# Performance work log

Hardware: AMD Instinct MI355X
Metric: run time of the kernel (lower is better)

Reference implementation:

```python
import jax, jax.numpy as jnp
import numpy as np

STD = 0.01

def setup_inputs() -> dict:
    key = jax.random.key(0)
    k1, k2, k3 = jax.random.split(key, 3)
    B, T, D = 16, 4096, 512
    x = jax.random.normal(k1, (B, T, D), dtype=jnp.float32)
    att_W = jax.random.normal(k2, (D, D), dtype=jnp.float32) * STD
    att_v = jax.random.normal(k3, (D,), dtype=jnp.float32) * STD
    return {"x": x, "att_W": att_W, "att_v": att_v}

def reference(x, att_W, att_v):
    # additive attention scores: tanh(x @ W) @ v -> [B, T]
    y = jnp.tanh(jnp.einsum('btd,de->bte', x, att_W))
    scores = jnp.einsum('btd,d->bt', y, att_v)
    weights = jax.nn.softmax(scores, axis=-1)          # softmax over sequence
    out = jnp.einsum('bt,btd->bd', weights, x)         # weighted sum pooling
    return out.astype(jnp.float32)
```

## Files before the change

### kernel.cpp

```cpp
#include <hip/hip_runtime.h>
#include <hip/hip_bf16.h>
#include <math.h>

#define BB 16
#define TT 4096
#define DD 512
#define MM (BB*TT)

typedef __bf16 bf16x8 __attribute__((ext_vector_type(8)));
typedef float  f32x4  __attribute__((ext_vector_type(4)));

__device__ inline unsigned short f2bf(float f) {
    unsigned u = __builtin_bit_cast(unsigned, f) + 0x8000u;
    return (unsigned short)(u >> 16);
}

__device__ inline unsigned pack_bf16x2(float lo, float hi) {
    unsigned u0 = __builtin_bit_cast(unsigned, lo) + 0x8000u;
    unsigned u1 = __builtin_bit_cast(unsigned, hi) + 0x8000u;
    return __builtin_amdgcn_perm(u1, u0, 0x07060302);
}

__device__ inline float tanh_fast(float y) {
    float e = __expf(2.0f * y);
    return 1.0f - 2.0f * __builtin_amdgcn_rcpf(e + 1.0f);
}

__global__ void wt_kernel(const float* __restrict__ W, unsigned short* __restrict__ Wt) {
    int idx = blockIdx.x * 256 + threadIdx.x;
    int n = idx >> 9;
    int k = idx & 511;
    Wt[idx] = f2bf(W[k * DD + n]);
}

__global__ __launch_bounds__(256, 2) void scores_kernel(
        const float* __restrict__ x, const unsigned short* __restrict__ Wt,
        const float* __restrict__ v, float* __restrict__ scores) {
    __shared__ unsigned short As[64 * DD];
    __shared__ float sbuf[4][64];

    const int tid  = threadIdx.x;
    const int m0   = blockIdx.x * 64;
    const int wid  = tid >> 6;
    const int lane = tid & 63;
    const int l15  = lane & 15;
    const int q    = lane >> 4;
    const int r3   = l15 & 7;

    const unsigned short* bbase = Wt + (size_t)(wid * 128 + l15) * DD + q * 8;
#define LOAD_B(p, ni, s) (*(const bf16x8*)(bbase + (size_t)((p) * 64 + (ni) * 16) * DD + (s) * 32))

    bf16x8 b[4][4];
    #pragma unroll
    for (int s = 0; s < 3; s++)
        #pragma unroll
        for (int ni = 0; ni < 4; ni++)
            b[s][ni] = LOAD_B(0, ni, s);

    #pragma unroll 4
    for (int i = 0; i < 16; i++) {
        int u = i * 256 + tid;
        int r = u >> 6;
        int c = u & 63;
        const float* gp = x + (size_t)(m0 + r) * DD + c * 8;
        float4 f0 = *(const float4*)(gp);
        float4 f1 = *(const float4*)(gp + 4);
        uint4 o;
        o.x = pack_bf16x2(f0.x, f0.y);
        o.y = pack_bf16x2(f0.z, f0.w);
        o.z = pack_bf16x2(f1.x, f1.y);
        o.w = pack_bf16x2(f1.z, f1.w);
        *(uint4*)(&As[r * DD + (c ^ (r & 7)) * 8]) = o;
    }
    __syncthreads();

    float vpart[4][4];
    #pragma unroll
    for (int mi = 0; mi < 4; mi++)
        #pragma unroll
        for (int rr = 0; rr < 4; rr++)
            vpart[mi][rr] = 0.f;

#define A_FRAG(mi, s) (*(const bf16x8*)(&As[((mi)*16 + l15) * DD + ((((s)*4 + q) ^ r3) * 8)]))

    #pragma unroll
    for (int p = 0; p < 2; p++) {
        if (p == 1) {
            #pragma unroll
            for (int s = 0; s < 3; s++)
                #pragma unroll
                for (int ni = 0; ni < 4; ni++)
                    b[s][ni] = LOAD_B(1, ni, s);
        }

        f32x4 acc[4][4];
        #pragma unroll
        for (int mi = 0; mi < 4; mi++)
            #pragma unroll
            for (int ni = 0; ni < 4; ni++)
                acc[mi][ni] = (f32x4){0.f, 0.f, 0.f, 0.f};

        bf16x8 a[2][4];
        #pragma unroll
        for (int mi = 0; mi < 4; mi++) a[0][mi] = A_FRAG(mi, 0);

        #pragma unroll
        for (int s = 0; s < 16; s++) {
            const int cur = s & 1;
            if (s < 15) {
                #pragma unroll
                for (int mi = 0; mi < 4; mi++) a[cur ^ 1][mi] = A_FRAG(mi, s + 1);
            }
            if (s < 13) {
                #pragma unroll
                for (int ni = 0; ni < 4; ni++)
                    b[(s + 3) & 3][ni] = LOAD_B(p, ni, s + 3);
            }
            #pragma unroll
            for (int mi = 0; mi < 4; mi++)
                #pragma unroll
                for (int ni = 0; ni < 4; ni++)
                    acc[mi][ni] = __builtin_amdgcn_mfma_f32_16x16x32_bf16(
                        a[cur][mi], b[s & 3][ni], acc[mi][ni], 0, 0, 0);
        }

        float vv[4];
        #pragma unroll
        for (int ni = 0; ni < 4; ni++)
            vv[ni] = v[wid * 128 + p * 64 + ni * 16 + l15];
        #pragma unroll
        for (int mi = 0; mi < 4; mi++)
            #pragma unroll
            for (int ni = 0; ni < 4; ni++)
                #pragma unroll
                for (int rr = 0; rr < 4; rr++)
                    vpart[mi][rr] += tanh_fast(acc[mi][ni][rr]) * vv[ni];
    }
#undef A_FRAG
#undef LOAD_B

    #pragma unroll
    for (int mi = 0; mi < 4; mi++)
        #pragma unroll
        for (int rr = 0; rr < 4; rr++) {
            float sum = vpart[mi][rr];
            sum += __shfl_xor(sum, 1);
            sum += __shfl_xor(sum, 2);
            sum += __shfl_xor(sum, 4);
            sum += __shfl_xor(sum, 8);
            if (l15 == 0)
                sbuf[wid][mi * 16 + q * 4 + rr] = sum;
        }
    __syncthreads();
    if (tid < 64)
        scores[m0 + tid] = sbuf[0][tid] + sbuf[1][tid] + sbuf[2][tid] + sbuf[3][tid];
}

__global__ void softmax_kernel(const float* __restrict__ scores, float* __restrict__ weights) {
    const int b = blockIdx.x;
    const int tid = threadIdx.x;
    __shared__ float wred[4];

    float s[16];
    float mx = -1e30f;
    #pragma unroll
    for (int i = 0; i < 16; i++) {
        float sv = scores[b * TT + i * 256 + tid];
        s[i] = sv;
        mx = fmaxf(mx, sv);
    }
    #pragma unroll
    for (int off = 32; off; off >>= 1) mx = fmaxf(mx, __shfl_xor(mx, off));
    if ((tid & 63) == 0) wred[tid >> 6] = mx;
    __syncthreads();
    mx = fmaxf(fmaxf(wred[0], wred[1]), fmaxf(wred[2], wred[3]));
    __syncthreads();

    float sum = 0.f;
    #pragma unroll
    for (int i = 0; i < 16; i++) { s[i] = __expf(s[i] - mx); sum += s[i]; }
    #pragma unroll
    for (int off = 32; off; off >>= 1) sum += __shfl_xor(sum, off);
    if ((tid & 63) == 0) wred[tid >> 6] = sum;
    __syncthreads();
    sum = wred[0] + wred[1] + wred[2] + wred[3];

    const float inv = 1.0f / sum;
    #pragma unroll
    for (int i = 0; i < 16; i++)
        weights[b * TT + i * 256 + tid] = s[i] * inv;
}

#define PTCH 256
__global__ void pool_kernel(const float* __restrict__ x, const float* __restrict__ weights,
                            float* __restrict__ out) {
    __shared__ float wsm[PTCH];
    const int b   = blockIdx.y;
    const int t0  = blockIdx.x * PTCH;
    const int tid = threadIdx.x;
    wsm[tid] = weights[b * TT + t0 + tid];
    __syncthreads();

    const int dq = tid & 127;
    const int ts = tid >> 7;
    f32x4 acc = (f32x4){0.f, 0.f, 0.f, 0.f};
    const float* xp = x + ((size_t)b * TT + t0) * DD + dq * 4;
    #pragma unroll 8
    for (int t = ts; t < PTCH; t += 2) {
        f32x4 xv = *(const f32x4*)(xp + (size_t)t * DD);
        float w = wsm[t];
        acc += w * xv;
    }
    float* op = out + b * DD + dq * 4;
    atomicAdd(op + 0, acc[0]);
    atomicAdd(op + 1, acc[1]);
    atomicAdd(op + 2, acc[2]);
    atomicAdd(op + 3, acc[3]);
}

extern "C" void kernel_launch(void* const* d_in, const int* in_sizes, int n_in,
                              void* d_out, int out_size, void* d_ws, size_t ws_size,
                              hipStream_t stream) {
    (void)in_sizes; (void)n_in; (void)out_size; (void)ws_size;
    const float* x = (const float*)d_in[0];
    const float* W = (const float*)d_in[1];
    const float* v = (const float*)d_in[2];
    float* out = (float*)d_out;

    unsigned short* Wt = (unsigned short*)d_ws;
    float* scores      = (float*)((char*)d_ws + 512 * 1024);
    float* weights     = (float*)((char*)d_ws + 512 * 1024 + 256 * 1024);

    hipMemsetAsync(d_out, 0, BB * DD * sizeof(float), stream);

    wt_kernel<<<DD * DD / 256, 256, 0, stream>>>(W, Wt);

    scores_kernel<<<MM / 64, 256, 0, stream>>>(x, Wt, v, scores);

    softmax_kernel<<<BB, 256, 0, stream>>>(scores, weights);

    pool_kernel<<<dim3(TT / PTCH, BB), 256, 0, stream>>>(x, weights, out);
}
```

Before: 303.8 us.

## Pre-pack W into MFMA fragment order and shrink pool tiles with in-block reduction

Weight preprocessing now writes W in bf16 already arranged in the per-lane MFMA B-fragment order, so each wave's B loads are fully contiguous 1KB chunks instead of strided row reads. Each wave now covers four 32-column panels instead of two 64-column ones, which halves the live accumulators and B registers and may ease register pressure. The pool kernel uses 64-row tiles, giving more blocks for better parallelism over x, and combines its two half-block partials in shared memory before issuing atomics, which halves the atomic traffic per block. The cost is more atomics overall across the additional pool blocks, plus an extra block-wide sync.

New measurement: 289.7 us. 1.05x faster.

```diff
diff --git a/kernel.cpp b/kernel.cpp
--- a/kernel.cpp
+++ b/kernel.cpp
@@ -26,15 +26,21 @@
     return 1.0f - 2.0f * __builtin_amdgcn_rcpf(e + 1.0f);
 }
 
-__global__ void wt_kernel(const float* __restrict__ W, unsigned short* __restrict__ Wt) {
-    int idx = blockIdx.x * 256 + threadIdx.x;
-    int n = idx >> 9;
-    int k = idx & 511;
-    Wt[idx] = f2bf(W[k * DD + n]);
+__global__ void wb_kernel(const float* __restrict__ W, unsigned short* __restrict__ Wb) {
+    int u = blockIdx.x * 256 + threadIdx.x;
+    int lane = u & 63;
+    int s  = (u >> 6) & 15;
+    int nf = u >> 10;
+    int n  = nf * 16 + (lane & 15);
+    int k0 = s * 32 + (lane >> 4) * 8;
+    unsigned short o[8];
+    #pragma unroll
+    for (int j = 0; j < 8; j++) o[j] = f2bf(W[(size_t)(k0 + j) * DD + n]);
+    *(uint4*)(Wb + (size_t)u * 8) = *(uint4*)o;
 }
 
 __global__ __launch_bounds__(256, 2) void scores_kernel(
-        const float* __restrict__ x, const unsigned short* __restrict__ Wt,
+        const float* __restrict__ x, const unsigned short* __restrict__ Wb,
         const float* __restrict__ v, float* __restrict__ scores) {
     __shared__ unsigned short As[64 * DD];
     __shared__ float sbuf[4][64];
@@ -47,15 +53,16 @@
     const int q    = lane >> 4;
     const int r3   = l15 & 7;
 
-    const unsigned short* bbase = Wt + (size_t)(wid * 128 + l15) * DD + q * 8;
-#define LOAD_B(p, ni, s) (*(const bf16x8*)(bbase + (size_t)((p) * 64 + (ni) * 16) * DD + (s) * 32))
-
-    bf16x8 b[4][4];
-    #pragma unroll
-    for (int s = 0; s < 3; s++)
-        #pragma unroll
-        for (int ni = 0; ni < 4; ni++)
-            b[s][ni] = LOAD_B(0, ni, s);
+    const unsigned short* bw = Wb + (size_t)lane * 8;
+#define BFRAG(p, ni, s) (*(const bf16x8*)(bw + ((size_t)((((p)*4 + wid)*2 + (ni))*16 + (s)) * 512)))
+#define A_FRAG(mi, s) (*(const bf16x8*)(&As[((mi)*16 + l15) * DD + ((((s)*4 + q) ^ r3) * 8)]))
+
+    bf16x8 b[4][2];
+    #pragma unroll
+    for (int s = 0; s < 3; s++) {
+        b[s][0] = BFRAG(0, 0, s);
+        b[s][1] = BFRAG(0, 1, s);
+    }
 
     #pragma unroll 4
     for (int i = 0; i < 16; i++) {
@@ -81,23 +88,21 @@
         for (int rr = 0; rr < 4; rr++)
             vpart[mi][rr] = 0.f;
 
-#define A_FRAG(mi, s) (*(const bf16x8*)(&As[((mi)*16 + l15) * DD + ((((s)*4 + q) ^ r3) * 8)]))
-
-    #pragma unroll
-    for (int p = 0; p < 2; p++) {
-        if (p == 1) {
-            #pragma unroll
-            for (int s = 0; s < 3; s++)
-                #pragma unroll
-                for (int ni = 0; ni < 4; ni++)
-                    b[s][ni] = LOAD_B(1, ni, s);
+    #pragma unroll
+    for (int p = 0; p < 4; p++) {
+        if (p > 0) {
+            #pragma unroll
+            for (int s = 0; s < 3; s++) {
+                b[s][0] = BFRAG(p, 0, s);
+                b[s][1] = BFRAG(p, 1, s);
+            }
         }
 
-        f32x4 acc[4][4];
+        f32x4 acc[4][2];
         #pragma unroll
         for (int mi = 0; mi < 4; mi++)
             #pragma unroll
-            for (int ni = 0; ni < 4; ni++)
+            for (int ni = 0; ni < 2; ni++)
                 acc[mi][ni] = (f32x4){0.f, 0.f, 0.f, 0.f};
 
         bf16x8 a[2][4];
@@ -112,32 +117,30 @@
                 for (int mi = 0; mi < 4; mi++) a[cur ^ 1][mi] = A_FRAG(mi, s + 1);
             }
             if (s < 13) {
-                #pragma unroll
-                for (int ni = 0; ni < 4; ni++)
-                    b[(s + 3) & 3][ni] = LOAD_B(p, ni, s + 3);
+                b[(s + 3) & 3][0] = BFRAG(p, 0, s + 3);
+                b[(s + 3) & 3][1] = BFRAG(p, 1, s + 3);
             }
             #pragma unroll
             for (int mi = 0; mi < 4; mi++)
                 #pragma unroll
-                for (int ni = 0; ni < 4; ni++)
+                for (int ni = 0; ni < 2; ni++)
                     acc[mi][ni] = __builtin_amdgcn_mfma_f32_16x16x32_bf16(
                         a[cur][mi], b[s & 3][ni], acc[mi][ni], 0, 0, 0);
         }
 
-        float vv[4];
-        #pragma unroll
-        for (int ni = 0; ni < 4; ni++)
-            vv[ni] = v[wid * 128 + p * 64 + ni * 16 + l15];
+        float vv[2];
+        vv[0] = v[(p * 4 + wid) * 32 + l15];
+        vv[1] = v[(p * 4 + wid) * 32 + 16 + l15];
         #pragma unroll
         for (int mi = 0; mi < 4; mi++)
             #pragma unroll
-            for (int ni = 0; ni < 4; ni++)
+            for (int ni = 0; ni < 2; ni++)
                 #pragma unroll
                 for (int rr = 0; rr < 4; rr++)
                     vpart[mi][rr] += tanh_fast(acc[mi][ni][rr]) * vv[ni];
     }
 #undef A_FRAG
-#undef LOAD_B
+#undef BFRAG
 
     #pragma unroll
     for (int mi = 0; mi < 4; mi++)
@@ -191,31 +194,38 @@
         weights[b * TT + i * 256 + tid] = s[i] * inv;
 }
 
-#define PTCH 256
-__global__ void pool_kernel(const float* __restrict__ x, const float* __restrict__ weights,
-                            float* __restrict__ out) {
+#define PTCH 64
+__global__ __launch_bounds__(256) void pool_kernel(
+        const float* __restrict__ x, const float* __restrict__ weights,
+        float* __restrict__ out) {
     __shared__ float wsm[PTCH];
+    __shared__ f32x4 psum[128];
     const int b   = blockIdx.y;
     const int t0  = blockIdx.x * PTCH;
     const int tid = threadIdx.x;
-    wsm[tid] = weights[b * TT + t0 + tid];
+    if (tid < PTCH) wsm[tid] = weights[b * TT + t0 + tid];
     __syncthreads();
 
     const int dq = tid & 127;
     const int ts = tid >> 7;
     f32x4 acc = (f32x4){0.f, 0.f, 0.f, 0.f};
-    const float* xp = x + ((size_t)b * TT + t0) * DD + dq * 4;
+    const float* xp = x + ((size_t)b * TT + t0 + ts) * DD + dq * 4;
     #pragma unroll 8
     for (int t = ts; t < PTCH; t += 2) {
-        f32x4 xv = *(const f32x4*)(xp + (size_t)t * DD);
-        float w = wsm[t];
-        acc += w * xv;
-    }
-    float* op = out + b * DD + dq * 4;
-    atomicAdd(op + 0, acc[0]);
-    atomicAdd(op + 1, acc[1]);
-    atomicAdd(op + 2, acc[2]);
-    atomicAdd(op + 3, acc[3]);
+        f32x4 xv = *(const f32x4*)xp;
+        acc += wsm[t] * xv;
+        xp += 2 * DD;
+    }
+    if (ts == 1) psum[dq] = acc;
+    __syncthreads();
+    if (ts == 0) {
+        acc += psum[dq];
+        float* op = out + b * DD + dq * 4;
+        atomicAdd(op + 0, acc[0]);
+        atomicAdd(op + 1, acc[1]);
+        atomicAdd(op + 2, acc[2]);
+        atomicAdd(op + 3, acc[3]);
+    }
 }
 
 extern "C" void kernel_launch(void* const* d_in, const int* in_sizes, int n_in,
@@ -227,15 +237,15 @@
     const float* v = (const float*)d_in[2];
     float* out = (float*)d_out;
 
-    unsigned short* Wt = (unsigned short*)d_ws;
+    unsigned short* Wb = (unsigned short*)d_ws;
     float* scores      = (float*)((char*)d_ws + 512 * 1024);
     float* weights     = (float*)((char*)d_ws + 512 * 1024 + 256 * 1024);
 
     hipMemsetAsync(d_out, 0, BB * DD * sizeof(float), stream);
 
-    wt_kernel<<<DD * DD / 256, 256, 0, stream>>>(W, Wt);
-
-    scores_kernel<<<MM / 64, 256, 0, stream>>>(x, Wt, v, scores);
+    wb_kernel<<<128, 256, 0, stream>>>(W, Wb);
+
+    scores_kernel<<<MM / 64, 256, 0, stream>>>(x, Wb, v, scores);
 
     softmax_kernel<<<BB, 256, 0, stream>>>(scores, weights);
 
```
